# Kernel tuning notes

Hardware: AMD Instinct MI355X
Metric: run time of the kernel (lower is better)

## Reference

```python
import jax, jax.numpy as jnp
import numpy as np

MIN_MZ, MAX_MZ, STEP = 0.0, 1000.0, 0.01
NUM_BINS = int((MAX_MZ - MIN_MZ) / STEP)      # 100000
GROUP_SIZE, OUT_PER_GROUP = 30, 3
GROUPS = NUM_BINS // GROUP_SIZE               # 3333
BINNER_OUT = GROUPS * OUT_PER_GROUP           # 9999
B, P = 256, 512


def setup_inputs() -> dict:
    key = jax.random.key(0)
    ks = jax.random.split(key, 16)
    mz1 = jax.random.uniform(ks[0], (B, P), jnp.float32) * 1000.0
    int1 = jax.random.uniform(ks[1], (B, P), jnp.float32)
    mz2 = jax.random.uniform(ks[2], (B, P), jnp.float32) * 1000.0
    int2 = jax.random.uniform(ks[3], (B, P), jnp.float32)

    def lin(k, fan_in, shape):
        return jax.random.normal(k, shape, jnp.float32) * (1.0 / np.sqrt(fan_in))

    Wg = lin(ks[4], GROUP_SIZE, (GROUPS, GROUP_SIZE, OUT_PER_GROUP))
    bg = jnp.zeros((GROUPS, OUT_PER_GROUP), jnp.float32)
    W1 = lin(ks[5], BINNER_OUT, (BINNER_OUT, 1000)); b1 = jnp.zeros((1000,), jnp.float32)
    W2 = lin(ks[6], 1000, (1000, 1000));             b2 = jnp.zeros((1000,), jnp.float32)
    W3 = lin(ks[7], 1000, (1000, 1000));             b3 = jnp.zeros((1000,), jnp.float32)
    Wo = lin(ks[8], 1000, (1000, 500));              bo = jnp.zeros((500,), jnp.float32)
    return {"mz1": mz1, "int1": int1, "mz2": mz2, "int2": int2,
            "Wg": Wg, "bg": bg, "W1": W1, "b1": b1, "W2": W2, "b2": b2,
            "W3": W3, "b3": b3, "Wo": Wo, "bo": bo}


def _bin_spectra(mz, inten):
    # histogram scatter-add: [B, P] peaks -> [B, NUM_BINS]
    idx = jnp.floor((mz - MIN_MZ) / STEP).astype(jnp.int32)
    valid = (mz >= MIN_MZ) & (mz < MAX_MZ)
    idx = jnp.clip(idx, 0, NUM_BINS - 1)
    vals = jnp.where(valid, inten, 0.0)
    out = jnp.zeros((mz.shape[0], NUM_BINS), inten.dtype)
    rows = jnp.arange(mz.shape[0])[:, None]
    return out.at[rows, idx].add(vals)


def _encode(mz, inten, Wg, bg, W1, b1, W2, b2, W3, b3, Wo, bo):
    x = _bin_spectra(mz, inten)                                # [B, NUM_BINS]
    xg = x[:, :GROUPS * GROUP_SIZE].reshape(-1, GROUPS, GROUP_SIZE)
    h = jnp.einsum('bgi,gio->bgo', xg, Wg) + bg                # grouped tiny linears
    h = h.reshape(-1, BINNER_OUT)
    h = jax.nn.relu(h @ W1 + b1)
    h = jax.nn.relu(h @ W2 + b2)
    h = jax.nn.relu(h @ W3 + b3)
    return h @ Wo + bo                                         # [B, 500]


def reference(mz1, int1, mz2, int2, Wg, bg, W1, b1, W2, b2, W3, b3, Wo, bo):
    e1 = _encode(mz1, int1, Wg, bg, W1, b1, W2, b2, W3, b3, Wo, bo)
    e2 = _encode(mz2, int2, Wg, bg, W1, b1, W2, b2, W3, b3, Wo, bo)
    eps = jnp.float32(1e-6)
    n1 = jnp.maximum(jnp.linalg.norm(e1, axis=1), eps)
    n2 = jnp.maximum(jnp.linalg.norm(e2, axis=1), eps)
    return jnp.sum(e1 * e2, axis=1) / (n1 * n2)
```

## Files before the change

### kernel.cpp

```cpp
#include <hip/hip_runtime.h>
#include <hip/hip_fp16.h>

using half8  = __attribute__((ext_vector_type(8))) _Float16;
using half4  = __attribute__((ext_vector_type(4))) _Float16;
using f32x4  = __attribute__((ext_vector_type(4))) float;

#define GROUPS      3333
#define BINNER_OUT  9999
#define BATCH       256
#define ROWS        512
#define PEAKS       512
#define K1          9999
#define K1P         10048
#define NP          1024
#define NOP         512
#define HALFK       5024

__device__ __forceinline__ void gl_lds16(const void* g, void* l) {
  __builtin_amdgcn_global_load_lds(
      (const __attribute__((address_space(1))) void*)g,
      (__attribute__((address_space(3))) void*)l, 16, 0, 0);
}

__device__ __forceinline__ void hs_add(float* p, float v) {
  __hip_atomic_fetch_add(p, v, __ATOMIC_RELAXED, __HIP_MEMORY_SCOPE_WORKGROUP);
}

__global__ __launch_bounds__(256) void prep4(
    const float* __restrict__ mz1, const float* __restrict__ it1,
    const float* __restrict__ mz2, const float* __restrict__ it2,
    const float* __restrict__ Wg,  const float* __restrict__ bg,
    _Float16* __restrict__ h16,
    const float* __restrict__ W1, _Float16* __restrict__ W1t,
    const float* __restrict__ W2, _Float16* __restrict__ W2t,
    const float* __restrict__ W3, _Float16* __restrict__ W3t,
    const float* __restrict__ Wo, _Float16* __restrict__ Wot) {
  __shared__ __align__(16) char smem[HALFK * 4];
  const int t = threadIdx.x;
  const int blk = blockIdx.x;

  if (blk < 1024) {
    float* hs = (float*)smem;
    const int row = blk >> 1, half = blk & 1;
    const int base = half * HALFK;
    const int s = row >> 8, b = row & 255;

    for (int k = t * 4; k < HALFK; k += 1024)
      *(f32x4*)&hs[k] = (f32x4){0.f, 0.f, 0.f, 0.f};
    __syncthreads();

    const float* mz = (s ? mz2 : mz1) + (size_t)b * PEAKS;
    const float* it = (s ? it2 : it1) + (size_t)b * PEAKS;

    float m[2], v[2], w[2][3]; int c0[2]; bool keep[2];
#pragma unroll
    for (int q = 0; q < 2; ++q) { m[q] = mz[t + q * 256]; v[q] = it[t + q * 256]; }
#pragma unroll
    for (int q = 0; q < 2; ++q) {
      bool val = (m[q] >= 0.0f && m[q] < 1000.0f);
      int bin = val ? (int)floorf(m[q] / 0.01f) : 0;
      bin = bin < 0 ? 0 : (bin > 99999 ? 99999 : bin);
      keep[q] = val && (bin < GROUPS * 30);
      int binL = bin < GROUPS * 30 ? bin : GROUPS * 30 - 1;
      const float* wp = Wg + (size_t)binL * 3;
      w[q][0] = wp[0]; w[q][1] = wp[1]; w[q][2] = wp[2];
      c0[q] = (bin / 30) * 3;
    }
#pragma unroll
    for (int q = 0; q < 2; ++q)
      if (keep[q]) {
#pragma unroll
        for (int o = 0; o < 3; ++o) {
          int c = c0[q] + o;
          if (c >= base && c < base + HALFK)
            hs_add(&hs[c - base], v[q] * w[q][o]);
        }
      }
    __syncthreads();

    _Float16* dst = h16 + (size_t)row * K1P + base;
    for (int k0 = t * 8; k0 < HALFK; k0 += 2048) {
      half8 vv;
#pragma unroll
      for (int j = 0; j < 8; ++j) {
        int c = base + k0 + j;
        float x = hs[k0 + j] + (c < BINNER_OUT ? bg[c] : 0.f);
        vv[j] = (_Float16)x;
      }
      *(half8*)(dst + k0) = vv;
    }
  } else {
    float (*tile)[66] = (float(*)[66])smem;
    int bid = blk - 1024;
    const float* W; _Float16* outp; int K, N, Kpad, g, in, ktiles;
    if (bid < 640)       { W = W1; outp = W1t; K = K1;   N = 1000; Kpad = K1P;
                           ktiles = 157; g = bid % 40; in = bid / 40; }
    else if (bid < 704)  { bid -= 640; W = W2; outp = W2t; K = 1000; N = 1000;
                           Kpad = NP; ktiles = 16; g = bid & 3; in = bid >> 2; }
    else if (bid < 768)  { bid -= 704; W = W3; outp = W3t; K = 1000; N = 1000;
                           Kpad = NP; ktiles = 16; g = bid & 3; in = bid >> 2; }
    else                 { bid -= 768; W = Wo; outp = Wot; K = 1000; N = 500;
                           Kpad = NP; ktiles = 16; g = bid & 3; in = bid >> 2; }
    const int ntile = min(4, ktiles - g * 4);
    const int k0base = g * 256, n0 = in * 64;
    const int r = t >> 2, cc = (t & 3) * 16;

    f32x4 cur[4], nxt[4];
    auto LOAD = [&](int i, f32x4* dst) {
      int k = k0base + i * 64 + r;
#pragma unroll
      for (int j = 0; j < 4; ++j) {
        int n = n0 + cc + j * 4;
        f32x4 v = (f32x4){0.f, 0.f, 0.f, 0.f};
        if (k < K && n < N)
          v = *(const f32x4*)(W + (size_t)k * N + n);
        dst[j] = v;
      }
    };

    LOAD(0, cur);
    for (int i = 0; i < ntile; ++i) {
      if (i) __syncthreads();
#pragma unroll
      for (int j = 0; j < 4; ++j) {
        tile[r][cc + j * 4 + 0] = cur[j][0];
        tile[r][cc + j * 4 + 1] = cur[j][1];
        tile[r][cc + j * 4 + 2] = cur[j][2];
        tile[r][cc + j * 4 + 3] = cur[j][3];
      }
      __syncthreads();
      if (i + 1 < ntile) LOAD(i + 1, nxt);
      const int k0 = k0base + i * 64;
#pragma unroll
      for (int h = 0; h < 2; ++h) {
        half8 v;
#pragma unroll
        for (int e = 0; e < 8; ++e) v[e] = (_Float16)tile[cc + h * 8 + e][r];
        *(half8*)(outp + (size_t)(n0 + r) * Kpad + k0 + cc + h * 8) = v;
      }
#pragma unroll
      for (int j = 0; j < 4; ++j) cur[j] = nxt[j];
    }
  }
}

template <bool SWZ>
__global__ __launch_bounds__(256) void gemm_sk(
    const _Float16* __restrict__ A, int lda,
    const _Float16* __restrict__ Bt, int ldb,
    float* __restrict__ part, int M, int Npad, int ksteps_total, int kspc) {
  __shared__ __align__(16) _Float16 As[3 * 4096];
  __shared__ __align__(16) _Float16 Bs[3 * 8192];

  int bx, by, bz;
  if (SWZ) {
    int bid = blockIdx.x;
    int xcd = bid & 7, i = bid >> 3;
    bz = i >> 3;
    int j = i & 7;
    bx = (xcd & 3) * 2 + (j & 1);
    by = (xcd >> 2) * 4 + (j >> 1);
  } else {
    bx = blockIdx.x; by = blockIdx.y; bz = blockIdx.z;
  }

  const int t = threadIdx.x, lane = t & 63, wid = t >> 6;
  const int m0 = by * 64, n0 = bx * 128;
  const int s0 = bz * kspc;
  const int s1 = min(s0 + kspc, ksteps_total);

  const int wr = wid >> 1, wc = wid & 1;
  const int r16 = lane & 15, kh = lane >> 4;

  const int lr  = lane >> 3;
  const int lkc = ((lane & 7) ^ lr) * 8;
  const _Float16* AgL = A  + (size_t)(m0 + wid * 16 + lr) * lda + lkc;
  const _Float16* BgL = Bt + (size_t)(n0 + wid * 32 + lr) * ldb + lkc;

  f32x4 acc[2][4] = {};

  auto STAGE = [&](int s, int buf) {
    const size_t ko = (size_t)s * 64;
    _Float16* ab = As + buf * 4096 + wid * 1024;
    _Float16* bb = Bs + buf * 8192 + wid * 2048;
    gl_lds16(AgL + ko,                     ab);
    gl_lds16(AgL + ko + (size_t) 8 * lda,  ab + 512);
    gl_lds16(BgL + ko,                     bb);
    gl_lds16(BgL + ko + (size_t) 8 * ldb,  bb + 512);
    gl_lds16(BgL + ko + (size_t)16 * ldb,  bb + 1024);
    gl_lds16(BgL + ko + (size_t)24 * ldb,  bb + 1536);
  };

  if (s0 < s1)     STAGE(s0, 0);
  if (s0 + 1 < s1) STAGE(s0 + 1, 1);

  int cur = 0;
  for (int s = s0; s < s1; ++s) {
    __builtin_amdgcn_s_barrier();
    const bool more2 = (s + 2 < s1), more1 = (s + 1 < s1);
    if (more2) STAGE(s + 2, cur == 0 ? 2 : (cur == 1 ? 0 : 1));
    if (more2)      asm volatile("s_waitcnt vmcnt(12)" ::: "memory");
    else if (more1) asm volatile("s_waitcnt vmcnt(6)"  ::: "memory");
    else            asm volatile("s_waitcnt vmcnt(0)"  ::: "memory");
    __builtin_amdgcn_s_barrier();

    const char* Ab = (const char*)(As + cur * 4096);
    const char* Bb = (const char*)(Bs + cur * 8192);
    half8 af[2][2], bf[4][2];
#pragma unroll
    for (int kc = 0; kc < 2; ++kc) {
#pragma unroll
      for (int mi = 0; mi < 2; ++mi) {
        int row = wr * 32 + mi * 16 + r16;
        af[mi][kc] = *(const half8*)(Ab + row * 128 +
                     (((kc << 6) + (kh << 4)) ^ ((row & 7) << 4)));
      }
#pragma unroll
      for (int ni = 0; ni < 4; ++ni) {
        int row = wc * 64 + ni * 16 + r16;
        bf[ni][kc] = *(const half8*)(Bb + row * 128 +
                     (((kc << 6) + (kh << 4)) ^ ((row & 7) << 4)));
      }
    }
#pragma unroll
    for (int kc = 0; kc < 2; ++kc)
#pragma unroll
      for (int mi = 0; mi < 2; ++mi)
#pragma unroll
        for (int ni = 0; ni < 4; ++ni)
          acc[mi][ni] = __builtin_amdgcn_mfma_f32_16x16x32_f16(
              af[mi][kc], bf[ni][kc], acc[mi][ni], 0, 0, 0);
    cur = cur == 2 ? 0 : cur + 1;
  }

  float* P = part + (size_t)bz * M * Npad;
#pragma unroll
  for (int mi = 0; mi < 2; ++mi)
#pragma unroll
    for (int ni = 0; ni < 4; ++ni) {
      int row = m0 + wr * 32 + mi * 16 + kh * 4;
      int col = n0 + wc * 64 + ni * 16 + r16;
#pragma unroll
      for (int rr = 0; rr < 4; ++rr)
        P[(size_t)(row + rr) * Npad + col] = acc[mi][ni][rr];
    }
}

__global__ void combine_sk(const float* __restrict__ part, int SK, int M, int Npad,
                           const float* __restrict__ bias, int Nreal,
                           _Float16* __restrict__ o16) {
  int i4 = (blockIdx.x * 256 + threadIdx.x) * 4;
  int total = M * Npad;
  if (i4 >= total) return;
  f32x4 s = (f32x4){0.f, 0.f, 0.f, 0.f};
  for (int zz = 0; zz < SK; ++zz)
    s += *(const f32x4*)&part[(size_t)zz * total + i4];
  int n = i4 & (Npad - 1);
  half4 v;
#pragma unroll
  for (int e = 0; e < 4; ++e) {
    float x = s[e] + ((n + e) < Nreal ? bias[n + e] : 0.f);
    v[e] = (_Float16)fmaxf(x, 0.f);
  }
  *(half4*)(o16 + i4) = v;
}

__global__ void combine_cos(const float* __restrict__ part,
                            const float* __restrict__ bo,
                            float* __restrict__ out) {
  const int b = blockIdx.x, t = threadIdx.x;
  float d = 0.f, s1 = 0.f, s2 = 0.f;
  for (int c = t; c < NOP; c += 256) {
    float e1 = 0.f, e2 = 0.f;
#pragma unroll
    for (int z = 0; z < 8; ++z) {
      e1 += part[((size_t)z * ROWS + b) * NOP + c];
      e2 += part[((size_t)z * ROWS + b + BATCH) * NOP + c];
    }
    if (c < 500) { float bb = bo[c]; e1 += bb; e2 += bb; }
    d += e1 * e2; s1 += e1 * e1; s2 += e2 * e2;
  }
  for (int off = 32; off > 0; off >>= 1) {
    d  += __shfl_down(d, off, 64);
    s1 += __shfl_down(s1, off, 64);
    s2 += __shfl_down(s2, off, 64);
  }
  __shared__ float rd[4], r1[4], r2[4];
  int wd = t >> 6, lane = t & 63;
  if (lane == 0) { rd[wd] = d; r1[wd] = s1; r2[wd] = s2; }
  __syncthreads();
  if (t == 0) {
    float D  = rd[0] + rd[1] + rd[2] + rd[3];
    float S1 = r1[0] + r1[1] + r1[2] + r1[3];
    float S2 = r2[0] + r2[1] + r2[2] + r2[3];
    float n1 = fmaxf(sqrtf(S1), 1e-6f);
    float n2 = fmaxf(sqrtf(S2), 1e-6f);
    out[b] = D / (n1 * n2);
  }
}

extern "C" void kernel_launch(void* const* d_in, const int* in_sizes, int n_in,
                              void* d_out, int out_size, void* d_ws, size_t ws_size,
                              hipStream_t stream) {
  const float* mz1 = (const float*)d_in[0];
  const float* it1 = (const float*)d_in[1];
  const float* mz2 = (const float*)d_in[2];
  const float* it2 = (const float*)d_in[3];
  const float* Wg  = (const float*)d_in[4];
  const float* bg  = (const float*)d_in[5];
  const float* W1  = (const float*)d_in[6];
  const float* b1  = (const float*)d_in[7];
  const float* W2  = (const float*)d_in[8];
  const float* b2  = (const float*)d_in[9];
  const float* W3  = (const float*)d_in[10];
  const float* b3  = (const float*)d_in[11];
  const float* Wo  = (const float*)d_in[12];
  const float* bo  = (const float*)d_in[13];
  float* out = (float*)d_out;

  char* ws = (char*)d_ws;
  size_t off = 0;
  auto take = [&](size_t bytes) {
    size_t o = off; off += (bytes + 255) & ~(size_t)255; return o;
  };
  float*    part = (float*)   (ws + take((size_t)8 * ROWS * NP * 4));
  _Float16* h16  = (_Float16*)(ws + take((size_t)ROWS * K1P * 2));
  _Float16* W1t  = (_Float16*)(ws + take((size_t)NP * K1P * 2));
  _Float16* W2t  = (_Float16*)(ws + take((size_t)NP * NP * 2));
  _Float16* W3t  = (_Float16*)(ws + take((size_t)NP * NP * 2));
  _Float16* Wot  = (_Float16*)(ws + take((size_t)NOP * NP * 2));
  _Float16* y1   = (_Float16*)(ws + take((size_t)ROWS * NP * 2));
  _Float16* y2   = (_Float16*)(ws + take((size_t)ROWS * NP * 2));
  _Float16* y3   = (_Float16*)(ws + take((size_t)ROWS * NP * 2));

  prep4<<<1824, 256, 0, stream>>>(mz1, it1, mz2, it2, Wg, bg, h16,
                                  W1, W1t, W2, W2t, W3, W3t, Wo, Wot);

  gemm_sk<true><<<512, 256, 0, stream>>>(
      h16, K1P, W1t, K1P, part, ROWS, NP, K1P / 64, 20);
  combine_sk<<<(ROWS * NP) / 1024, 256, 0, stream>>>(part, 8, ROWS, NP, b1, 1000, y1);

  gemm_sk<true><<<512, 256, 0, stream>>>(
      y1, NP, W2t, NP, part, ROWS, NP, NP / 64, 2);
  combine_sk<<<(ROWS * NP) / 1024, 256, 0, stream>>>(part, 8, ROWS, NP, b2, 1000, y2);

  gemm_sk<true><<<512, 256, 0, stream>>>(
      y2, NP, W3t, NP, part, ROWS, NP, NP / 64, 2);
  combine_sk<<<(ROWS * NP) / 1024, 256, 0, stream>>>(part, 8, ROWS, NP, b3, 1000, y3);

  gemm_sk<false><<<dim3(NOP / 128, ROWS / 64, 8), 256, 0, stream>>>(
      y3, NP, Wot, NP, part, ROWS, NOP, NP / 64, 2);

  combine_cos<<<BATCH, 256, 0, stream>>>(part, bo, out);
}
```

Measured before the change: 97.52 us.

## Fuse binning, weight transpose and first GEMM into a flag-synchronised persistent kernel

Merges the prep kernel and the first split-K GEMM into one 512-block kernel. Each block bins one whole spectrum row, then transposes weight tiles, signalling completion through per-row-group and per-column-group atomic counters. Blocks then spin-wait only on the flags they depend on before running their GEMM tile, so one kernel launch and the full device-wide barrier between prep and GEMM1 go away. The risks are deadlock if not all 512 blocks are co-resident (launch bounds request 2 blocks per CU), spin and fence overhead, and larger LDS use per block.

Result: slower. 224.1 us (+129.8%).

```diff
diff --git a/kernel.cpp b/kernel.cpp
--- a/kernel.cpp
+++ b/kernel.cpp
@@ -14,7 +14,6 @@
 #define K1P         10048
 #define NP          1024
 #define NOP         512
-#define HALFK       5024
 
 __device__ __forceinline__ void gl_lds16(const void* g, void* l) {
   __builtin_amdgcn_global_load_lds(
@@ -26,7 +25,11 @@
   __hip_atomic_fetch_add(p, v, __ATOMIC_RELAXED, __HIP_MEMORY_SCOPE_WORKGROUP);
 }
 
-__global__ __launch_bounds__(256) void prep4(
+__global__ void init_flags(unsigned* f) {
+  if (threadIdx.x < 32) f[threadIdx.x] = 0u;
+}
+
+__global__ __launch_bounds__(256, 2) void mega(
     const float* __restrict__ mz1, const float* __restrict__ it1,
     const float* __restrict__ mz2, const float* __restrict__ it2,
     const float* __restrict__ Wg,  const float* __restrict__ bg,
@@ -34,24 +37,21 @@
     const float* __restrict__ W1, _Float16* __restrict__ W1t,
     const float* __restrict__ W2, _Float16* __restrict__ W2t,
     const float* __restrict__ W3, _Float16* __restrict__ W3t,
-    const float* __restrict__ Wo, _Float16* __restrict__ Wot) {
-  __shared__ __align__(16) char smem[HALFK * 4];
+    const float* __restrict__ Wo, _Float16* __restrict__ Wot,
+    float* __restrict__ part, unsigned* __restrict__ flags) {
+  __shared__ __align__(16) char smem[73728];
   const int t = threadIdx.x;
-  const int blk = blockIdx.x;
-
-  if (blk < 1024) {
+  const int bid = blockIdx.x;
+
+  {
     float* hs = (float*)smem;
-    const int row = blk >> 1, half = blk & 1;
-    const int base = half * HALFK;
-    const int s = row >> 8, b = row & 255;
-
-    for (int k = t * 4; k < HALFK; k += 1024)
+    const int s = bid >> 8, b = bid & 255;
+    for (int k = t * 4; k < K1P; k += 1024)
       *(f32x4*)&hs[k] = (f32x4){0.f, 0.f, 0.f, 0.f};
     __syncthreads();
 
     const float* mz = (s ? mz2 : mz1) + (size_t)b * PEAKS;
     const float* it = (s ? it2 : it1) + (size_t)b * PEAKS;
-
     float m[2], v[2], w[2][3]; int c0[2]; bool keep[2];
 #pragma unroll
     for (int q = 0; q < 2; ++q) { m[q] = mz[t + q * 256]; v[q] = it[t + q * 256]; }
@@ -70,57 +70,58 @@
     for (int q = 0; q < 2; ++q)
       if (keep[q]) {
 #pragma unroll
-        for (int o = 0; o < 3; ++o) {
-          int c = c0[q] + o;
-          if (c >= base && c < base + HALFK)
-            hs_add(&hs[c - base], v[q] * w[q][o]);
-        }
+        for (int o = 0; o < 3; ++o) hs_add(&hs[c0[q] + o], v[q] * w[q][o]);
       }
     __syncthreads();
 
-    _Float16* dst = h16 + (size_t)row * K1P + base;
-    for (int k0 = t * 8; k0 < HALFK; k0 += 2048) {
+    _Float16* dst = h16 + (size_t)bid * K1P;
+    for (int k0 = t * 8; k0 < K1P; k0 += 2048) {
       half8 vv;
 #pragma unroll
       for (int j = 0; j < 8; ++j) {
-        int c = base + k0 + j;
-        float x = hs[k0 + j] + (c < BINNER_OUT ? bg[c] : 0.f);
+        int c = k0 + j;
+        float x = hs[c] + (c < BINNER_OUT ? bg[c] : 0.f);
         vv[j] = (_Float16)x;
       }
       *(half8*)(dst + k0) = vv;
     }
-  } else {
+  }
+  __syncthreads();
+  if (t == 0) {
+    __builtin_amdgcn_fence(__ATOMIC_RELEASE, "agent");
+    __hip_atomic_fetch_add(&flags[bid >> 6], 1u, __ATOMIC_ACQ_REL,
+                           __HIP_MEMORY_SCOPE_AGENT);
+  }
+
+  for (int g = bid; g < 800; g += 512) {
     float (*tile)[66] = (float(*)[66])smem;
-    int bid = blk - 1024;
-    const float* W; _Float16* outp; int K, N, Kpad, g, in, ktiles;
-    if (bid < 640)       { W = W1; outp = W1t; K = K1;   N = 1000; Kpad = K1P;
-                           ktiles = 157; g = bid % 40; in = bid / 40; }
-    else if (bid < 704)  { bid -= 640; W = W2; outp = W2t; K = 1000; N = 1000;
-                           Kpad = NP; ktiles = 16; g = bid & 3; in = bid >> 2; }
-    else if (bid < 768)  { bid -= 704; W = W3; outp = W3t; K = 1000; N = 1000;
-                           Kpad = NP; ktiles = 16; g = bid & 3; in = bid >> 2; }
-    else                 { bid -= 768; W = Wo; outp = Wot; K = 1000; N = 500;
-                           Kpad = NP; ktiles = 16; g = bid & 3; in = bid >> 2; }
-    const int ntile = min(4, ktiles - g * 4);
-    const int k0base = g * 256, n0 = in * 64;
+    const float* W; _Float16* outp; int K, N, Kpad, kg, in, ktiles;
+    if (g < 640)      { W = W1; outp = W1t; K = K1;   N = 1000; Kpad = K1P;
+                        ktiles = 157; kg = g % 40; in = g / 40; }
+    else if (g < 704) { int lb = g - 640; W = W2; outp = W2t; K = 1000; N = 1000;
+                        Kpad = NP; ktiles = 16; kg = lb & 3; in = lb >> 2; }
+    else if (g < 768) { int lb = g - 704; W = W3; outp = W3t; K = 1000; N = 1000;
+                        Kpad = NP; ktiles = 16; kg = lb & 3; in = lb >> 2; }
+    else              { int lb = g - 768; W = Wo; outp = Wot; K = 1000; N = 500;
+                        Kpad = NP; ktiles = 16; kg = lb & 3; in = lb >> 2; }
+    const int ntile = min(4, ktiles - kg * 4);
+    const int k0base = kg * 256, n0 = in * 64;
     const int r = t >> 2, cc = (t & 3) * 16;
 
     f32x4 cur[4], nxt[4];
-    auto LOAD = [&](int i, f32x4* dst) {
+    auto LOAD = [&](int i, f32x4* d) {
       int k = k0base + i * 64 + r;
 #pragma unroll
       for (int j = 0; j < 4; ++j) {
         int n = n0 + cc + j * 4;
         f32x4 v = (f32x4){0.f, 0.f, 0.f, 0.f};
-        if (k < K && n < N)
-          v = *(const f32x4*)(W + (size_t)k * N + n);
-        dst[j] = v;
+        if (k < K && n < N) v = *(const f32x4*)(W + (size_t)k * N + n);
+        d[j] = v;
       }
     };
-
     LOAD(0, cur);
     for (int i = 0; i < ntile; ++i) {
-      if (i) __syncthreads();
+      __syncthreads();
 #pragma unroll
       for (int j = 0; j < 4; ++j) {
         tile[r][cc + j * 4 + 0] = cur[j][0];
@@ -141,6 +142,111 @@
 #pragma unroll
       for (int j = 0; j < 4; ++j) cur[j] = nxt[j];
     }
+    __syncthreads();
+    if (t == 0 && g < 640) {
+      __builtin_amdgcn_fence(__ATOMIC_RELEASE, "agent");
+      __hip_atomic_fetch_add(&flags[8 + g / 40], 1u, __ATOMIC_ACQ_REL,
+                             __HIP_MEMORY_SCOPE_AGENT);
+    }
+  }
+
+  int xcd = bid & 7, i2 = bid >> 3;
+  const int bz = i2 >> 3;
+  int j2 = i2 & 7;
+  const int bx = (xcd & 3) * 2 + (j2 & 1);
+  const int by = (xcd >> 2) * 4 + (j2 >> 1);
+
+  if (t == 0) {
+    while (__hip_atomic_load(&flags[by], __ATOMIC_ACQUIRE,
+                             __HIP_MEMORY_SCOPE_AGENT) < 64u ||
+           __hip_atomic_load(&flags[8 + 2 * bx], __ATOMIC_ACQUIRE,
+                             __HIP_MEMORY_SCOPE_AGENT) < 40u ||
+           __hip_atomic_load(&flags[8 + 2 * bx + 1], __ATOMIC_ACQUIRE,
+                             __HIP_MEMORY_SCOPE_AGENT) < 40u)
+      __builtin_amdgcn_s_sleep(2);
+  }
+  __syncthreads();
+  __builtin_amdgcn_fence(__ATOMIC_ACQUIRE, "agent");
+
+  {
+    _Float16* As = (_Float16*)smem;
+    _Float16* Bs = (_Float16*)(smem + 24576);
+    const int lane = t & 63, wid = t >> 6;
+    const int m0 = by * 64, n0 = bx * 128;
+    const int s0 = bz * 20;
+    const int s1 = min(s0 + 20, 157);
+    const int wr = wid >> 1, wc = wid & 1;
+    const int r16 = lane & 15, kh = lane >> 4;
+    const int lr  = lane >> 3;
+    const int lkc = ((lane & 7) ^ lr) * 8;
+    const _Float16* AgL = h16 + (size_t)(m0 + wid * 16 + lr) * K1P + lkc;
+    const _Float16* BgL = W1t + (size_t)(n0 + wid * 32 + lr) * K1P + lkc;
+
+    f32x4 acc[2][4] = {};
+    auto STAGE = [&](int s, int buf) {
+      const size_t ko = (size_t)s * 64;
+      _Float16* ab = As + buf * 4096 + wid * 1024;
+      _Float16* bb = Bs + buf * 8192 + wid * 2048;
+      gl_lds16(AgL + ko,                    ab);
+      gl_lds16(AgL + ko + (size_t) 8 * K1P, ab + 512);
+      gl_lds16(BgL + ko,                    bb);
+      gl_lds16(BgL + ko + (size_t) 8 * K1P, bb + 512);
+      gl_lds16(BgL + ko + (size_t)16 * K1P, bb + 1024);
+      gl_lds16(BgL + ko + (size_t)24 * K1P, bb + 1536);
+    };
+    STAGE(s0, 0);
+    STAGE(s0 + 1, 1);
+
+    int cur = 0;
+    for (int s = s0; s < s1; ++s) {
+      __builtin_amdgcn_s_barrier();
+      const bool more2 = (s + 2 < s1), more1 = (s + 1 < s1);
+      if (more2) STAGE(s + 2, cur == 0 ? 2 : (cur == 1 ? 0 : 1));
+      if (more2)      asm volatile("s_waitcnt vmcnt(12)" ::: "memory");
+      else if (more1) asm volatile("s_waitcnt vmcnt(6)"  ::: "memory");
+      else            asm volatile("s_waitcnt vmcnt(0)"  ::: "memory");
+      __builtin_amdgcn_s_barrier();
+
+      const char* Ab = (const char*)(As + cur * 4096);
+      const char* Bb = (const char*)(Bs + cur * 8192);
+      half8 af[2][2], bf[4][2];
+#pragma unroll
+      for (int kc = 0; kc < 2; ++kc) {
+#pragma unroll
+        for (int mi = 0; mi < 2; ++mi) {
+          int row = wr * 32 + mi * 16 + r16;
+          af[mi][kc] = *(const half8*)(Ab + row * 128 +
+                       (((kc << 6) + (kh << 4)) ^ ((row & 7) << 4)));
+        }
+#pragma unroll
+        for (int ni = 0; ni < 4; ++ni) {
+          int row = wc * 64 + ni * 16 + r16;
+          bf[ni][kc] = *(const half8*)(Bb + row * 128 +
+                       (((kc << 6) + (kh << 4)) ^ ((row & 7) << 4)));
+        }
+      }
+#pragma unroll
+      for (int kc = 0; kc < 2; ++kc)
+#pragma unroll
+        for (int mi = 0; mi < 2; ++mi)
+#pragma unroll
+          for (int ni = 0; ni < 4; ++ni)
+            acc[mi][ni] = __builtin_amdgcn_mfma_f32_16x16x32_f16(
+                af[mi][kc], bf[ni][kc], acc[mi][ni], 0, 0, 0);
+      cur = cur == 2 ? 0 : cur + 1;
+    }
+
+    float* P = part + (size_t)bz * ROWS * NP;
+#pragma unroll
+    for (int mi = 0; mi < 2; ++mi)
+#pragma unroll
+      for (int ni = 0; ni < 4; ++ni) {
+        int row = m0 + wr * 32 + mi * 16 + kh * 4;
+        int col = n0 + wc * 64 + ni * 16 + r16;
+#pragma unroll
+        for (int rr = 0; rr < 4; ++rr)
+          P[(size_t)(row + rr) * NP + col] = acc[mi][ni][rr];
+      }
   }
 }
 
@@ -168,17 +274,14 @@
   const int m0 = by * 64, n0 = bx * 128;
   const int s0 = bz * kspc;
   const int s1 = min(s0 + kspc, ksteps_total);
-
   const int wr = wid >> 1, wc = wid & 1;
   const int r16 = lane & 15, kh = lane >> 4;
-
   const int lr  = lane >> 3;
   const int lkc = ((lane & 7) ^ lr) * 8;
   const _Float16* AgL = A  + (size_t)(m0 + wid * 16 + lr) * lda + lkc;
   const _Float16* BgL = Bt + (size_t)(n0 + wid * 32 + lr) * ldb + lkc;
 
   f32x4 acc[2][4] = {};
-
   auto STAGE = [&](int s, int buf) {
     const size_t ko = (size_t)s * 64;
     _Float16* ab = As + buf * 4096 + wid * 1024;
@@ -323,21 +426,22 @@
   auto take = [&](size_t bytes) {
     size_t o = off; off += (bytes + 255) & ~(size_t)255; return o;
   };
-  float*    part = (float*)   (ws + take((size_t)8 * ROWS * NP * 4));
-  _Float16* h16  = (_Float16*)(ws + take((size_t)ROWS * K1P * 2));
-  _Float16* W1t  = (_Float16*)(ws + take((size_t)NP * K1P * 2));
-  _Float16* W2t  = (_Float16*)(ws + take((size_t)NP * NP * 2));
-  _Float16* W3t  = (_Float16*)(ws + take((size_t)NP * NP * 2));
-  _Float16* Wot  = (_Float16*)(ws + take((size_t)NOP * NP * 2));
-  _Float16* y1   = (_Float16*)(ws + take((size_t)ROWS * NP * 2));
-  _Float16* y2   = (_Float16*)(ws + take((size_t)ROWS * NP * 2));
-  _Float16* y3   = (_Float16*)(ws + take((size_t)ROWS * NP * 2));
-
-  prep4<<<1824, 256, 0, stream>>>(mz1, it1, mz2, it2, Wg, bg, h16,
-                                  W1, W1t, W2, W2t, W3, W3t, Wo, Wot);
-
-  gemm_sk<true><<<512, 256, 0, stream>>>(
-      h16, K1P, W1t, K1P, part, ROWS, NP, K1P / 64, 20);
+  float*    part  = (float*)   (ws + take((size_t)8 * ROWS * NP * 4));
+  _Float16* h16   = (_Float16*)(ws + take((size_t)ROWS * K1P * 2));
+  _Float16* W1t   = (_Float16*)(ws + take((size_t)NP * K1P * 2));
+  _Float16* W2t   = (_Float16*)(ws + take((size_t)NP * NP * 2));
+  _Float16* W3t   = (_Float16*)(ws + take((size_t)NP * NP * 2));
+  _Float16* Wot   = (_Float16*)(ws + take((size_t)NOP * NP * 2));
+  _Float16* y1    = (_Float16*)(ws + take((size_t)ROWS * NP * 2));
+  _Float16* y2    = (_Float16*)(ws + take((size_t)ROWS * NP * 2));
+  _Float16* y3    = (_Float16*)(ws + take((size_t)ROWS * NP * 2));
+  unsigned* flags = (unsigned*)(ws + take(128));
+
+  init_flags<<<1, 64, 0, stream>>>(flags);
+
+  mega<<<512, 256, 0, stream>>>(mz1, it1, mz2, it2, Wg, bg, h16,
+                                W1, W1t, W2, W2t, W3, W3t, Wo, Wot,
+                                part, flags);
   combine_sk<<<(ROWS * NP) / 1024, 256, 0, stream>>>(part, 8, ROWS, NP, b1, 1000, y1);
 
   gemm_sk<true><<<512, 256, 0, stream>>>(
```

## Replace split-K gemms for small layers with full-K gemms fusing bias and ReLU

Applied to the files above, without the earlier changes.

Layers 2, 3 and the output layer previously used 8-way split-K gemms writing fp32 partials, followed by separate combine kernels. They now use a full-K 64x64-tile gemm that applies bias, ReLU and fp16 conversion in its epilogue. The final layer writes fp32 embeddings directly, and a simplified cosine kernel reads them. This removes partial-buffer round trips and three kernel launches, but the grids drop to 128 and 64 blocks with a longer serial K loop, leaving many CUs idle.

Result: faster. 89.26 us (-8.5%).

```diff
diff --git a/kernel.cpp b/kernel.cpp
--- a/kernel.cpp
+++ b/kernel.cpp
@@ -171,14 +171,12 @@
 
   const int wr = wid >> 1, wc = wid & 1;
   const int r16 = lane & 15, kh = lane >> 4;
-
   const int lr  = lane >> 3;
   const int lkc = ((lane & 7) ^ lr) * 8;
   const _Float16* AgL = A  + (size_t)(m0 + wid * 16 + lr) * lda + lkc;
   const _Float16* BgL = Bt + (size_t)(n0 + wid * 32 + lr) * ldb + lkc;
 
   f32x4 acc[2][4] = {};
-
   auto STAGE = [&](int s, int buf) {
     const size_t ko = (size_t)s * 64;
     _Float16* ab = As + buf * 4096 + wid * 1024;
@@ -246,6 +244,95 @@
     }
 }
 
+template <int RELU>
+__global__ __launch_bounds__(256) void gemm_full(
+    const _Float16* __restrict__ A,
+    const _Float16* __restrict__ Bt,
+    const float* __restrict__ bias, int Nreal, int Npad,
+    _Float16* __restrict__ o16, float* __restrict__ o32) {
+  __shared__ __align__(16) _Float16 As[3 * 4096];
+  __shared__ __align__(16) _Float16 Bs[3 * 4096];
+
+  const int bx = blockIdx.x, by = blockIdx.y;
+  const int t = threadIdx.x, lane = t & 63, wid = t >> 6;
+  const int m0 = by * 64, n0 = bx * 64;
+  const int wr = wid >> 1, wc = wid & 1;
+  const int r16 = lane & 15, kh = lane >> 4;
+  const int lr  = lane >> 3;
+  const int lkc = ((lane & 7) ^ lr) * 8;
+  const _Float16* AgL = A  + (size_t)(m0 + wid * 16 + lr) * NP + lkc;
+  const _Float16* BgL = Bt + (size_t)(n0 + wid * 16 + lr) * NP + lkc;
+
+  f32x4 acc[2][2] = {};
+  auto STAGE = [&](int s, int buf) {
+    const size_t ko = (size_t)s * 64;
+    _Float16* ab = As + buf * 4096 + wid * 1024;
+    _Float16* bb = Bs + buf * 4096 + wid * 1024;
+    gl_lds16(AgL + ko,                    ab);
+    gl_lds16(AgL + ko + (size_t)8 * NP,   ab + 512);
+    gl_lds16(BgL + ko,                    bb);
+    gl_lds16(BgL + ko + (size_t)8 * NP,   bb + 512);
+  };
+
+  STAGE(0, 0);
+  STAGE(1, 1);
+
+  int cur = 0;
+  for (int s = 0; s < 16; ++s) {
+    __builtin_amdgcn_s_barrier();
+    const bool more2 = (s + 2 < 16), more1 = (s + 1 < 16);
+    if (more2) STAGE(s + 2, cur == 0 ? 2 : (cur == 1 ? 0 : 1));
+    if (more2)      asm volatile("s_waitcnt vmcnt(8)" ::: "memory");
+    else if (more1) asm volatile("s_waitcnt vmcnt(4)" ::: "memory");
+    else            asm volatile("s_waitcnt vmcnt(0)" ::: "memory");
+    __builtin_amdgcn_s_barrier();
+
+    const char* Ab = (const char*)(As + cur * 4096);
+    const char* Bb = (const char*)(Bs + cur * 4096);
+    half8 af[2][2], bf[2][2];
+#pragma unroll
+    for (int kc = 0; kc < 2; ++kc) {
+#pragma unroll
+      for (int mi = 0; mi < 2; ++mi) {
+        int row = wr * 32 + mi * 16 + r16;
+        af[mi][kc] = *(const half8*)(Ab + row * 128 +
+                     (((kc << 6) + (kh << 4)) ^ ((row & 7) << 4)));
+      }
+#pragma unroll
+      for (int ni = 0; ni < 2; ++ni) {
+        int row = wc * 32 + ni * 16 + r16;
+        bf[ni][kc] = *(const half8*)(Bb + row * 128 +
+                     (((kc << 6) + (kh << 4)) ^ ((row & 7) << 4)));
+      }
+    }
+#pragma unroll
+    for (int kc = 0; kc < 2; ++kc)
+#pragma unroll
+      for (int mi = 0; mi < 2; ++mi)
+#pragma unroll
+        for (int ni = 0; ni < 2; ++ni)
+          acc[mi][ni] = __builtin_amdgcn_mfma_f32_16x16x32_f16(
+              af[mi][kc], bf[ni][kc], acc[mi][ni], 0, 0, 0);
+    cur = cur == 2 ? 0 : cur + 1;
+  }
+
+#pragma unroll
+  for (int mi = 0; mi < 2; ++mi)
+#pragma unroll
+    for (int ni = 0; ni < 2; ++ni) {
+      int row = m0 + wr * 32 + mi * 16 + kh * 4;
+      int col = n0 + wc * 32 + ni * 16 + r16;
+      float bb = (col < Nreal) ? bias[col] : 0.f;
+#pragma unroll
+      for (int rr = 0; rr < 4; ++rr) {
+        float x = acc[mi][ni][rr] + bb;
+        if (RELU) x = fmaxf(x, 0.f);
+        if (o16) o16[(size_t)(row + rr) * Npad + col] = (_Float16)x;
+        else     o32[(size_t)(row + rr) * Npad + col] = x;
+      }
+    }
+}
+
 __global__ void combine_sk(const float* __restrict__ part, int SK, int M, int Npad,
                            const float* __restrict__ bias, int Nreal,
                            _Float16* __restrict__ o16) {
@@ -265,19 +352,12 @@
   *(half4*)(o16 + i4) = v;
 }
 
-__global__ void combine_cos(const float* __restrict__ part,
-                            const float* __restrict__ bo,
-                            float* __restrict__ out) {
+__global__ void cosine_E(const float* __restrict__ E, float* __restrict__ out) {
   const int b = blockIdx.x, t = threadIdx.x;
   float d = 0.f, s1 = 0.f, s2 = 0.f;
   for (int c = t; c < NOP; c += 256) {
-    float e1 = 0.f, e2 = 0.f;
-#pragma unroll
-    for (int z = 0; z < 8; ++z) {
-      e1 += part[((size_t)z * ROWS + b) * NOP + c];
-      e2 += part[((size_t)z * ROWS + b + BATCH) * NOP + c];
-    }
-    if (c < 500) { float bb = bo[c]; e1 += bb; e2 += bb; }
+    float e1 = E[(size_t)b * NOP + c];
+    float e2 = E[(size_t)(b + BATCH) * NOP + c];
     d += e1 * e2; s1 += e1 * e1; s2 += e2 * e2;
   }
   for (int off = 32; off > 0; off >>= 1) {
@@ -332,6 +412,7 @@
   _Float16* y1   = (_Float16*)(ws + take((size_t)ROWS * NP * 2));
   _Float16* y2   = (_Float16*)(ws + take((size_t)ROWS * NP * 2));
   _Float16* y3   = (_Float16*)(ws + take((size_t)ROWS * NP * 2));
+  float*    E    = (float*)   (ws + take((size_t)ROWS * NOP * 4));
 
   prep4<<<1824, 256, 0, stream>>>(mz1, it1, mz2, it2, Wg, bg, h16,
                                   W1, W1t, W2, W2t, W3, W3t, Wo, Wot);
@@ -340,16 +421,12 @@
       h16, K1P, W1t, K1P, part, ROWS, NP, K1P / 64, 20);
   combine_sk<<<(ROWS * NP) / 1024, 256, 0, stream>>>(part, 8, ROWS, NP, b1, 1000, y1);
 
-  gemm_sk<true><<<512, 256, 0, stream>>>(
-      y1, NP, W2t, NP, part, ROWS, NP, NP / 64, 2);
-  combine_sk<<<(ROWS * NP) / 1024, 256, 0, stream>>>(part, 8, ROWS, NP, b2, 1000, y2);
-
-  gemm_sk<true><<<512, 256, 0, stream>>>(
-      y2, NP, W3t, NP, part, ROWS, NP, NP / 64, 2);
-  combine_sk<<<(ROWS * NP) / 1024, 256, 0, stream>>>(part, 8, ROWS, NP, b3, 1000, y3);
-
-  gemm_sk<false><<<dim3(NOP / 128, ROWS / 64, 8), 256, 0, stream>>>(
-      y3, NP, Wot, NP, part, ROWS, NOP, NP / 64, 2);
-
-  combine_cos<<<BATCH, 256, 0, stream>>>(part, bo, out);
-}
+  gemm_full<1><<<dim3(NP / 64, ROWS / 64), 256, 0, stream>>>(
+      y1, W2t, b2, 1000, NP, y2, nullptr);
+  gemm_full<1><<<dim3(NP / 64, ROWS / 64), 256, 0, stream>>>(
+      y2, W3t, b3, 1000, NP, y3, nullptr);
+  gemm_full<0><<<dim3(NOP / 64, ROWS / 64), 256, 0, stream>>>(
+      y3, Wot, bo, 500, NOP, nullptr, E);
+
+  cosine_E<<<BATCH, 256, 0, stream>>>(E, out);
+}
```
